# Performance work log

Hardware: AMD Instinct MI355X
Metric: run time of the kernel (lower is better)

The kernel has to match this reference:

```python
import jax, jax.numpy as jnp
import numpy as np

EPS = 1e-6
N_REP = 4  # num_heads // num_kv_heads


def _qk_norm(a):
    a32 = a.astype(jnp.float32)
    var = jnp.mean(jnp.square(a32), axis=-1, keepdims=True)
    return (a32 * jax.lax.rsqrt(var + EPS)).astype(a.dtype)


def setup_inputs() -> dict:
    key = jax.random.key(0)
    ks = jax.random.split(key, 5)
    B, Tq, C, H, D, Hkv = 2, 2048, 2048, 16, 128, 4
    s = 0.02
    return {
        "x_q": jax.random.normal(ks[0], (B, Tq, C), dtype=jnp.float32),
        "Wq": jax.random.normal(ks[1], (C, H, D), dtype=jnp.float32) * s,
        "Wk": jax.random.normal(ks[2], (C, Hkv, D), dtype=jnp.float32) * s,
        "Wv": jax.random.normal(ks[3], (C, Hkv, D), dtype=jnp.float32) * s,
        "Wo": jax.random.normal(ks[4], (H * D, C), dtype=jnp.float32) * s,
    }


def reference(x_q, Wq, Wk, Wv, Wo):
    # x_q: (B, Tq, C); self-attention (x_kv = x_q)
    B, Tq, C = x_q.shape
    D = Wq.shape[-1]
    q = jnp.einsum('btc,chd->bthd', x_q, Wq)   # (B,Tq,H,D)
    k = jnp.einsum('btc,chd->bthd', x_q, Wk)   # (B,Tq,Hkv,D)
    v = jnp.einsum('btc,chd->bthd', x_q, Wv)
    # per-head QK RMS-norm
    q = _qk_norm(q)
    k = _qk_norm(k)
    # GQA: repeat kv heads (each kv head repeated N_REP times consecutively)
    k = jnp.repeat(k, N_REP, axis=2)           # (B,Tq,H,D)
    v = jnp.repeat(v, N_REP, axis=2)
    scale = jnp.asarray(1.0 / np.sqrt(D), dtype=q.dtype)
    logits = jnp.einsum('bqhd,bkhd->bhqk', q, k) * scale
    attn = jax.nn.softmax(logits, axis=-1)
    out = jnp.einsum('bhqk,bkhd->bqhd', attn, v)
    out = out.reshape(B, Tq, -1)               # (B,Tq,H*D)
    return out @ Wo                            # (B,Tq,C)
```

## Files before the change

kernel.cpp:

```cpp
#include <hip/hip_runtime.h>

typedef __attribute__((ext_vector_type(4))) float f32x4;
typedef __attribute__((ext_vector_type(16))) float f32x16;
typedef __attribute__((ext_vector_type(8))) short bf16x8;
typedef __attribute__((ext_vector_type(4))) unsigned u32x4;

#define DEV __device__ __forceinline__

DEV unsigned short f2bf(float f) {
  unsigned u = __float_as_uint(f);
  unsigned r = (u + 0x7FFFu + ((u >> 16) & 1u)) >> 16;
  return (unsigned short)r;
}
DEV float bf2f(unsigned short h) { return __uint_as_float(((unsigned)h) << 16); }

DEV unsigned cvtpk(float lo, float hi) {
  unsigned r;
  asm("v_cvt_pk_bf16_f32 %0, %1, %2" : "=v"(r) : "v"(lo), "v"(hi));
  return r;
}
DEV bf16x8 frag4(unsigned a, unsigned b, unsigned c, unsigned d) {
  u32x4 u = {a, b, c, d};
  return __builtin_bit_cast(bf16x8, u);
}

typedef __attribute__((address_space(1))) void gas_t;
typedef __attribute__((address_space(3))) void las_t;
DEV void async16(void* lds, const void* g) {
  __builtin_amdgcn_global_load_lds((gas_t*)g, (las_t*)lds, 16, 0, 0);
}

__global__ void cast_x(const float* __restrict__ x, unsigned short* __restrict__ y, int n8) {
  int idx = blockIdx.x * blockDim.x + threadIdx.x;
  int stride = gridDim.x * blockDim.x;
  for (; idx < n8; idx += stride) {
    const float4* p = (const float4*)(x + (size_t)idx * 8);
    float4 v0 = p[0], v1 = p[1];
    bf16x8 o;
    o[0] = (short)f2bf(v0.x); o[1] = (short)f2bf(v0.y);
    o[2] = (short)f2bf(v0.z); o[3] = (short)f2bf(v0.w);
    o[4] = (short)f2bf(v1.x); o[5] = (short)f2bf(v1.y);
    o[6] = (short)f2bf(v1.z); o[7] = (short)f2bf(v1.w);
    *(bf16x8*)(y + (size_t)idx * 8) = o;
  }
}

__global__ void transpose_cast(const float* __restrict__ W, unsigned short* __restrict__ Wt,
                               int Kdim, int Nw) {
  __shared__ float tile[32][33];
  int n0 = blockIdx.x * 32, k0 = blockIdx.y * 32;
  int tx = threadIdx.x, ty = threadIdx.y;
#pragma unroll
  for (int r = ty; r < 32; r += 8)
    tile[r][tx] = W[(size_t)(k0 + r) * Nw + n0 + tx];
  __syncthreads();
#pragma unroll
  for (int r = ty; r < 32; r += 8)
    Wt[(size_t)(n0 + r) * Kdim + k0 + tx] = f2bf(tile[tx][r]);
}

template <int EPI>
__global__ __launch_bounds__(256, 2)
void gemm_bt(const unsigned short* __restrict__ A, const unsigned short* __restrict__ Bt,
             int Kr, float* __restrict__ Cf, int Nr,
             unsigned short* __restrict__ Qn, unsigned short* __restrict__ Kn,
             unsigned short* __restrict__ Vt) {
  __shared__ __align__(16) unsigned short lsA[128 * 32];
  __shared__ __align__(16) unsigned short lsB[128 * 32];
  const int t = threadIdx.x;
  const int lane = t & 63;
  const int w = t >> 6, wr = w >> 1, wc = w & 1;
  const int lo = lane & 15, hi = lane >> 4;
  const int m0 = blockIdx.y * 128, n0 = blockIdx.x * 128;

  const int c0 = t, c1 = t + 256;
  const unsigned short* gA0 = A + (size_t)(m0 + (c0 >> 2)) * Kr + (c0 & 3) * 8;
  const unsigned short* gA1 = A + (size_t)(m0 + (c1 >> 2)) * Kr + (c1 & 3) * 8;
  const unsigned short* gB0 = Bt + (size_t)(n0 + (c0 >> 2)) * Kr + (c0 & 3) * 8;
  const unsigned short* gB1 = Bt + (size_t)(n0 + (c1 >> 2)) * Kr + (c1 & 3) * 8;
  unsigned short* lA0 = lsA + c0 * 8;
  unsigned short* lA1 = lsA + c1 * 8;
  unsigned short* lB0 = lsB + c0 * 8;
  unsigned short* lB1 = lsB + c1 * 8;

  f32x4 acc[4][4] = {};

  for (int kt = 0; kt < Kr; kt += 32) {
    async16(lA0, gA0 + kt);
    async16(lA1, gA1 + kt);
    async16(lB0, gB0 + kt);
    async16(lB1, gB1 + kt);
    __syncthreads();
    bf16x8 af[4], bfr[4];
#pragma unroll
    for (int i = 0; i < 4; ++i) {
      af[i]  = *(const bf16x8*)&lsA[(wr * 64 + i * 16 + lo) * 32 + hi * 8];
      bfr[i] = *(const bf16x8*)&lsB[(wc * 64 + i * 16 + lo) * 32 + hi * 8];
    }
#pragma unroll
    for (int mi = 0; mi < 4; ++mi)
#pragma unroll
      for (int ni = 0; ni < 4; ++ni)
        acc[mi][ni] = __builtin_amdgcn_mfma_f32_16x16x32_bf16(af[mi], bfr[ni], acc[mi][ni], 0, 0, 0);
    __syncthreads();
  }

#pragma unroll
  for (int mi = 0; mi < 4; ++mi)
#pragma unroll
    for (int ni = 0; ni < 4; ++ni)
#pragma unroll
      for (int i = 0; i < 4; ++i) {
        int gm = m0 + wr * 64 + mi * 16 + hi * 4 + i;
        int gn = n0 + wc * 64 + ni * 16 + lo;
        float v = acc[mi][ni][i];
        if (EPI == 0) {
          Cf[(size_t)gm * Nr + gn] = v;
        } else {
          unsigned short bv = f2bf(v);
          int bb = gm >> 11, tt = gm & 2047;
          if (gn < 2048) {
            int hh = gn >> 7, dd = gn & 127;
            Qn[(((size_t)bb * 16 + hh) * 2048 + tt) * 128 + dd] = bv;
          } else if (gn < 2560) {
            int g2 = gn - 2048, hh = g2 >> 7, dd = g2 & 127;
            Kn[(((size_t)bb * 4 + hh) * 2048 + tt) * 128 + dd] = bv;
          } else {
            int g2 = gn - 2560, hh = g2 >> 7, dd = g2 & 127;
            Vt[(((size_t)bb * 4 + hh) * 128 + dd) * 2048 + tt] = bv;
          }
        }
      }
}

__global__ __launch_bounds__(256)
void qk_norm(unsigned short* __restrict__ Qn, unsigned short* __restrict__ Kn, float qscale) {
  int row = blockIdx.x * 4 + (threadIdx.x >> 6);
  int lane = threadIdx.x & 63;
  unsigned short* base;
  float scl;
  if (row < 65536) { base = Qn + (size_t)row * 128; scl = qscale; }
  else             { base = Kn + (size_t)(row - 65536) * 128; scl = 1.0f; }
  unsigned v = *(const unsigned*)(base + lane * 2);
  float a = bf2f((unsigned short)(v & 0xffffu));
  float b = bf2f((unsigned short)(v >> 16));
  float ss = a * a + b * b;
#pragma unroll
  for (int m = 1; m < 64; m <<= 1) ss += __shfl_xor(ss, m, 64);
  float r = rsqrtf(ss * (1.0f / 128.0f) + 1e-6f) * scl;
  *(unsigned*)(base + lane * 2) = ((unsigned)f2bf(b * r) << 16) | (unsigned)f2bf(a * r);
}

__global__ __launch_bounds__(256, 2)
void attn(const unsigned short* __restrict__ Q, const unsigned short* __restrict__ Kk,
          const unsigned short* __restrict__ Vt, unsigned short* __restrict__ AO) {
  const int bid = blockIdx.x;
  const int bh = (bid & 7) + 8 * (bid >> 7);
  const int qx = (bid >> 3) & 15;
  const int b = bh >> 4, h = bh & 15;
  const int hkv = h >> 2;
  const int t = threadIdx.x;
  const int w = t >> 6, lane = t & 63;
  const int qi = lane & 31, h1 = lane >> 5;
  const unsigned short* Qb = Q  + (size_t)bh * 2048 * 128;
  const unsigned short* Kb = Kk + (size_t)(b * 4 + hkv) * 2048 * 128;
  const unsigned short* Vb = Vt + (size_t)(b * 4 + hkv) * 128 * 2048;
  const int q0 = qx * 128 + w * 32;

  __shared__ __align__(16) unsigned short Klds[2][64 * 128];
  __shared__ __align__(16) unsigned short Vlds[2][128 * 64];

  bf16x8 qf[8];
#pragma unroll
  for (int s = 0; s < 8; ++s)
    qf[s] = *(const bf16x8*)&Qb[(size_t)(q0 + qi) * 128 + s * 16 + h1 * 8];

  f32x16 Oc[4] = {};
  float mrow = -1e30f, srow = 0.f;

#define STAGE_KV(bufi, kt_)                                                      \
  {                                                                              \
    const unsigned short* gK = Kb + (size_t)(kt_) * 128;                         \
    const unsigned short* gV = Vb + (kt_);                                       \
    _Pragma("unroll")                                                            \
    for (int j = 0; j < 4; ++j) {                                                \
      int gi = j * 256 + t;                                                      \
      int kr = gi >> 4, kg = (gi & 15) ^ (kr & 15);                              \
      async16(&Klds[bufi][gi * 8], gK + (size_t)kr * 128 + kg * 8);              \
      int vr = gi >> 3, vg = (gi & 7) ^ (vr & 7);                                \
      async16(&Vlds[bufi][gi * 8], gV + (size_t)vr * 2048 + vg * 8);             \
    }                                                                            \
  }

  STAGE_KV(0, 0);
  __syncthreads();

  int cur = 0;
  for (int kt = 0; kt < 2048; kt += 64) {
    if (kt + 64 < 2048) STAGE_KV(cur ^ 1, kt + 64);

    const unsigned short* KL = Klds[cur];
    const unsigned short* VL = Vlds[cur];

    f32x16 S[2] = {};
    __builtin_amdgcn_s_setprio(1);
#pragma unroll
    for (int mt = 0; mt < 2; ++mt) {
      const int krow = mt * 32 + qi;
      const unsigned short* krp = KL + krow * 128;
      const int rswz = krow & 15;
#pragma unroll
      for (int s = 0; s < 8; ++s) {
        bf16x8 kf = *(const bf16x8*)(krp + (((2 * s + h1) ^ rswz) << 3));
        S[mt] = __builtin_amdgcn_mfma_f32_32x32x16_bf16(kf, qf[s], S[mt], 0, 0, 0);
      }
    }
    __builtin_amdgcn_s_setprio(0);

    float t8[8];
#pragma unroll
    for (int r = 0; r < 8; ++r)
      t8[r] = fmaxf(fmaxf(S[0][r], S[0][r + 8]), fmaxf(S[1][r], S[1][r + 8]));
#pragma unroll
    for (int r = 0; r < 4; ++r) t8[r] = fmaxf(t8[r], t8[r + 4]);
    float mx = fmaxf(fmaxf(t8[0], t8[1]), fmaxf(t8[2], t8[3]));
    mx = fmaxf(mx, __shfl_xor(mx, 32, 64));
    if (__any(mx > mrow + 8.0f)) {
      float mnew = fmaxf(mrow, mx);
      float al = __builtin_amdgcn_exp2f(mrow - mnew);
      mrow = mnew;
      srow *= al;
#pragma unroll
      for (int dt = 0; dt < 4; ++dt)
#pragma unroll
        for (int r = 0; r < 16; ++r) Oc[dt][r] *= al;
    }
#pragma unroll
    for (int mt = 0; mt < 2; ++mt)
#pragma unroll
      for (int r = 0; r < 16; ++r)
        S[mt][r] = __builtin_amdgcn_exp2f(S[mt][r] - mrow);
    float s8[8];
#pragma unroll
    for (int r = 0; r < 8; ++r)
      s8[r] = (S[0][r] + S[0][r + 8]) + (S[1][r] + S[1][r + 8]);
#pragma unroll
    for (int r = 0; r < 4; ++r) s8[r] += s8[r + 4];
    float rs = (s8[0] + s8[1]) + (s8[2] + s8[3]);
    rs += __shfl_xor(rs, 32, 64);
    srow += rs;

    __builtin_amdgcn_s_setprio(1);
#pragma unroll
    for (int mt = 0; mt < 2; ++mt) {
      unsigned wd[8];
#pragma unroll
      for (int i2 = 0; i2 < 8; ++i2) wd[i2] = cvtpk(S[mt][2 * i2], S[mt][2 * i2 + 1]);
      unsigned r0 = __shfl_xor(h1 ? wd[0] : wd[2], 32, 64);
      unsigned r1 = __shfl_xor(h1 ? wd[1] : wd[3], 32, 64);
      unsigned r2 = __shfl_xor(h1 ? wd[4] : wd[6], 32, 64);
      unsigned r3 = __shfl_xor(h1 ? wd[5] : wd[7], 32, 64);
      bf16x8 pf0 = frag4(h1 ? r0 : wd[0], h1 ? r1 : wd[1], h1 ? wd[2] : r0, h1 ? wd[3] : r1);
      bf16x8 pf1 = frag4(h1 ? r2 : wd[4], h1 ? r3 : wd[5], h1 ? wd[6] : r2, h1 ? wd[7] : r3);
#pragma unroll
      for (int dt = 0; dt < 4; ++dt) {
        const int vrow = dt * 32 + qi;
        const unsigned short* vrp = VL + vrow * 64;
        const int vswz = vrow & 7;
        bf16x8 v0 = *(const bf16x8*)(vrp + (((mt * 4 + 0 + h1) ^ vswz) << 3));
        bf16x8 v1 = *(const bf16x8*)(vrp + (((mt * 4 + 2 + h1) ^ vswz) << 3));
        Oc[dt] = __builtin_amdgcn_mfma_f32_32x32x16_bf16(v0, pf0, Oc[dt], 0, 0, 0);
        Oc[dt] = __builtin_amdgcn_mfma_f32_32x32x16_bf16(v1, pf1, Oc[dt], 0, 0, 0);
      }
    }
    __builtin_amdgcn_s_setprio(0);

    __syncthreads();
    cur ^= 1;
  }

  const float inv = 1.0f / srow;
  const size_t orow = ((size_t)(b * 2048 + q0 + qi)) * 2048 + h * 128;
#pragma unroll
  for (int dt = 0; dt < 4; ++dt)
#pragma unroll
    for (int rq = 0; rq < 4; ++rq) {
      int d0 = dt * 32 + 8 * rq + 4 * h1;
      unsigned u0 = cvtpk(Oc[dt][4 * rq + 0] * inv, Oc[dt][4 * rq + 1] * inv);
      unsigned u1 = cvtpk(Oc[dt][4 * rq + 2] * inv, Oc[dt][4 * rq + 3] * inv);
      uint2 st = {u0, u1};
      *(uint2*)((unsigned short*)AO + orow + d0) = st;
    }
}

extern "C" void kernel_launch(void* const* d_in, const int* in_sizes, int n_in,
                              void* d_out, int out_size, void* d_ws, size_t ws_size,
                              hipStream_t stream) {
  const float* x_q = (const float*)d_in[0];
  const float* Wq  = (const float*)d_in[1];
  const float* Wk  = (const float*)d_in[2];
  const float* Wv  = (const float*)d_in[3];
  const float* Wo  = (const float*)d_in[4];
  float* out = (float*)d_out;

  char* ws = (char*)d_ws;
  unsigned short* Xb    = (unsigned short*)(ws);
  unsigned short* WqkvT = (unsigned short*)(ws + 16777216);
  unsigned short* WoT   = (unsigned short*)(ws + 29360128);
  unsigned short* Qn    = (unsigned short*)(ws + 37748736);
  unsigned short* Kn    = (unsigned short*)(ws + 54525952);
  unsigned short* Vt    = (unsigned short*)(ws + 58720256);
  unsigned short* AO    = Xb;

  cast_x<<<2048, 256, 0, stream>>>(x_q, Xb, (4096 * 2048) / 8);
  transpose_cast<<<dim3(2048 / 32, 2048 / 32), dim3(32, 8), 0, stream>>>(Wq, WqkvT, 2048, 2048);
  transpose_cast<<<dim3(512 / 32, 2048 / 32), dim3(32, 8), 0, stream>>>(Wk, WqkvT + 2048 * 2048, 2048, 512);
  transpose_cast<<<dim3(512 / 32, 2048 / 32), dim3(32, 8), 0, stream>>>(Wv, WqkvT + 2560 * 2048, 2048, 512);
  transpose_cast<<<dim3(2048 / 32, 2048 / 32), dim3(32, 8), 0, stream>>>(Wo, WoT, 2048, 2048);

  gemm_bt<1><<<dim3(3072 / 128, 4096 / 128), 256, 0, stream>>>(Xb, WqkvT, 2048, nullptr, 0, Qn, Kn, Vt);
  qk_norm<<<(65536 + 16384) / 4, 256, 0, stream>>>(Qn, Kn, 0.12751742f);
  attn<<<512, 256, 0, stream>>>(Qn, Kn, Vt, AO);
  gemm_bt<0><<<dim3(2048 / 128, 4096 / 128), 256, 0, stream>>>(AO, WoT, 2048, out, 2048,
                                                               nullptr, nullptr, nullptr);
}
```

Baseline: 240.4 us.

## Pre-arrange V into MFMA fragment layout and load directly from global

Adds a fragV kernel that rewrites V into per-lane MFMA fragment order, so the attention kernel reads V fragments straight from global memory into registers instead of staging them through LDS. The attention block mapping is also changed so the four query heads sharing one KV head run together, and the GEMM tiles are remapped with an XCD-aware swizzle. These aim to cut LDS traffic and improve L2 reuse. The cost is an extra kernel launch and pass over V, plus more register pressure and exposed global load latency in the attention loop.

Measured after the change: 255.9 us. 1.06x slower.

```diff
diff --git a/kernel.cpp b/kernel.cpp
--- a/kernel.cpp
+++ b/kernel.cpp
@@ -71,7 +71,10 @@
   const int lane = t & 63;
   const int w = t >> 6, wr = w >> 1, wc = w & 1;
   const int lo = lane & 15, hi = lane >> 4;
-  const int m0 = blockIdx.y * 128, n0 = blockIdx.x * 128;
+  const int nwg = gridDim.x * 32;
+  const int bid0 = blockIdx.y * gridDim.x + blockIdx.x;
+  const int sw = (bid0 & 7) * (nwg >> 3) + (bid0 >> 3);
+  const int m0 = (sw & 31) * 128, n0 = (sw >> 5) * 128;
 
   const int c0 = t, c1 = t + 256;
   const unsigned short* gA0 = A + (size_t)(m0 + (c0 >> 2)) * Kr + (c0 & 3) * 8;
@@ -151,24 +154,37 @@
   *(unsigned*)(base + lane * 2) = ((unsigned)f2bf(b * r) << 16) | (unsigned)f2bf(a * r);
 }
 
+__global__ __launch_bounds__(256)
+void fragV(const unsigned short* __restrict__ Vt, unsigned short* __restrict__ Vf) {
+  int tid = blockIdx.x * 256 + threadIdx.x;
+  int bhkv = tid >> 15, c = tid & 32767;
+  int lane = c & 63, tile = c >> 10, mid = (c >> 6) & 15;
+  int dt = mid >> 2, g2 = mid & 3;
+  int d = dt * 32 + (lane & 31);
+  int g = g2 * 2 + (lane >> 5);
+  int k0 = tile * 64 + g * 8;
+  const uint4* src = (const uint4*)(Vt + ((size_t)bhkv * 128 + d) * 2048 + k0);
+  uint4* dst = (uint4*)(Vf + (size_t)bhkv * 262144 + (size_t)c * 8);
+  *dst = *src;
+}
+
 __global__ __launch_bounds__(256, 2)
 void attn(const unsigned short* __restrict__ Q, const unsigned short* __restrict__ Kk,
-          const unsigned short* __restrict__ Vt, unsigned short* __restrict__ AO) {
+          const unsigned short* __restrict__ Vf, unsigned short* __restrict__ AO) {
   const int bid = blockIdx.x;
-  const int bh = (bid & 7) + 8 * (bid >> 7);
-  const int qx = (bid >> 3) & 15;
-  const int b = bh >> 4, h = bh & 15;
-  const int hkv = h >> 2;
+  const int x = bid & 7, r2 = bid >> 3;
+  const int h2 = r2 & 3, qx = r2 >> 2;
+  const int b = x >> 2, hkv = x & 3;
+  const int h = hkv * 4 + h2, bh = b * 16 + h, bhkv = b * 4 + hkv;
   const int t = threadIdx.x;
   const int w = t >> 6, lane = t & 63;
   const int qi = lane & 31, h1 = lane >> 5;
   const unsigned short* Qb = Q  + (size_t)bh * 2048 * 128;
-  const unsigned short* Kb = Kk + (size_t)(b * 4 + hkv) * 2048 * 128;
-  const unsigned short* Vb = Vt + (size_t)(b * 4 + hkv) * 128 * 2048;
+  const unsigned short* Kb = Kk + (size_t)bhkv * 2048 * 128;
+  const unsigned short* Vfb = Vf + (size_t)bhkv * 262144;
   const int q0 = qx * 128 + w * 32;
 
   __shared__ __align__(16) unsigned short Klds[2][64 * 128];
-  __shared__ __align__(16) unsigned short Vlds[2][128 * 64];
 
   bf16x8 qf[8];
 #pragma unroll
@@ -178,29 +194,35 @@
   f32x16 Oc[4] = {};
   float mrow = -1e30f, srow = 0.f;
 
-#define STAGE_KV(bufi, kt_)                                                      \
+#define STAGE_K(bufi, kt_)                                                       \
   {                                                                              \
     const unsigned short* gK = Kb + (size_t)(kt_) * 128;                         \
-    const unsigned short* gV = Vb + (kt_);                                       \
     _Pragma("unroll")                                                            \
     for (int j = 0; j < 4; ++j) {                                                \
       int gi = j * 256 + t;                                                      \
       int kr = gi >> 4, kg = (gi & 15) ^ (kr & 15);                              \
       async16(&Klds[bufi][gi * 8], gK + (size_t)kr * 128 + kg * 8);              \
-      int vr = gi >> 3, vg = (gi & 7) ^ (vr & 7);                                \
-      async16(&Vlds[bufi][gi * 8], gV + (size_t)vr * 2048 + vg * 8);             \
     }                                                                            \
   }
 
-  STAGE_KV(0, 0);
+  STAGE_K(0, 0);
   __syncthreads();
 
   int cur = 0;
-  for (int kt = 0; kt < 2048; kt += 64) {
-    if (kt + 64 < 2048) STAGE_KV(cur ^ 1, kt + 64);
+  for (int ti = 0; ti < 32; ++ti) {
+    if (ti + 1 < 32) STAGE_K(cur ^ 1, (ti + 1) * 64);
+
+    bf16x8 vf0[2][4], vf1[2][4];
+#pragma unroll
+    for (int mt = 0; mt < 2; ++mt)
+#pragma unroll
+      for (int dt = 0; dt < 4; ++dt) {
+        const unsigned short* vp = Vfb + ((size_t)((ti * 4 + dt) * 4 + mt * 2)) * 512 + lane * 8;
+        vf0[mt][dt] = *(const bf16x8*)(vp);
+        vf1[mt][dt] = *(const bf16x8*)(vp + 512);
+      }
 
     const unsigned short* KL = Klds[cur];
-    const unsigned short* VL = Vlds[cur];
 
     f32x16 S[2] = {};
     __builtin_amdgcn_s_setprio(1);
@@ -258,19 +280,14 @@
       for (int i2 = 0; i2 < 8; ++i2) wd[i2] = cvtpk(S[mt][2 * i2], S[mt][2 * i2 + 1]);
       unsigned r0 = __shfl_xor(h1 ? wd[0] : wd[2], 32, 64);
       unsigned r1 = __shfl_xor(h1 ? wd[1] : wd[3], 32, 64);
-      unsigned r2 = __shfl_xor(h1 ? wd[4] : wd[6], 32, 64);
+      unsigned r2_ = __shfl_xor(h1 ? wd[4] : wd[6], 32, 64);
       unsigned r3 = __shfl_xor(h1 ? wd[5] : wd[7], 32, 64);
       bf16x8 pf0 = frag4(h1 ? r0 : wd[0], h1 ? r1 : wd[1], h1 ? wd[2] : r0, h1 ? wd[3] : r1);
-      bf16x8 pf1 = frag4(h1 ? r2 : wd[4], h1 ? r3 : wd[5], h1 ? wd[6] : r2, h1 ? wd[7] : r3);
+      bf16x8 pf1 = frag4(h1 ? r2_ : wd[4], h1 ? r3 : wd[5], h1 ? wd[6] : r2_, h1 ? wd[7] : r3);
 #pragma unroll
       for (int dt = 0; dt < 4; ++dt) {
-        const int vrow = dt * 32 + qi;
-        const unsigned short* vrp = VL + vrow * 64;
-        const int vswz = vrow & 7;
-        bf16x8 v0 = *(const bf16x8*)(vrp + (((mt * 4 + 0 + h1) ^ vswz) << 3));
-        bf16x8 v1 = *(const bf16x8*)(vrp + (((mt * 4 + 2 + h1) ^ vswz) << 3));
-        Oc[dt] = __builtin_amdgcn_mfma_f32_32x32x16_bf16(v0, pf0, Oc[dt], 0, 0, 0);
-        Oc[dt] = __builtin_amdgcn_mfma_f32_32x32x16_bf16(v1, pf1, Oc[dt], 0, 0, 0);
+        Oc[dt] = __builtin_amdgcn_mfma_f32_32x32x16_bf16(vf0[mt][dt], pf0, Oc[dt], 0, 0, 0);
+        Oc[dt] = __builtin_amdgcn_mfma_f32_32x32x16_bf16(vf1[mt][dt], pf1, Oc[dt], 0, 0, 0);
       }
     }
     __builtin_amdgcn_s_setprio(0);
@@ -311,6 +328,7 @@
   unsigned short* Kn    = (unsigned short*)(ws + 54525952);
   unsigned short* Vt    = (unsigned short*)(ws + 58720256);
   unsigned short* AO    = Xb;
+  unsigned short* Vf    = WqkvT;
 
   cast_x<<<2048, 256, 0, stream>>>(x_q, Xb, (4096 * 2048) / 8);
   transpose_cast<<<dim3(2048 / 32, 2048 / 32), dim3(32, 8), 0, stream>>>(Wq, WqkvT, 2048, 2048);
@@ -320,7 +338,8 @@
 
   gemm_bt<1><<<dim3(3072 / 128, 4096 / 128), 256, 0, stream>>>(Xb, WqkvT, 2048, nullptr, 0, Qn, Kn, Vt);
   qk_norm<<<(65536 + 16384) / 4, 256, 0, stream>>>(Qn, Kn, 0.12751742f);
-  attn<<<512, 256, 0, stream>>>(Qn, Kn, Vt, AO);
+  fragV<<<1024, 256, 0, stream>>>(Vt, Vf);
+  attn<<<512, 256, 0, stream>>>(Qn, Kn, Vf, AO);
   gemm_bt<0><<<dim3(2048 / 128, 4096 / 128), 256, 0, stream>>>(AO, WoT, 2048, out, 2048,
                                                                nullptr, nullptr, nullptr);
 }
```

## Fuse QK RMS-norm into QKV GEMM epilogue and swizzle block mapping

Applied to the files above, without the earlier changes.

Removes the separate qk_norm kernel by computing per-row sums of squares in the QKV GEMM epilogue. A 128-wide output tile covers exactly one head, so the reduction uses lane shuffles plus a cross-wave LDS exchange, and the normalized, scaled values are written straight out as bf16. This drops a full read/write pass over Q and K plus one launch, and normalizes from fp32 accumulators instead of rounded bf16. It also adds an XCD-style block-index swizzle that remaps tiles across the grid for cache locality, at the cost of a hardcoded 32-row-tile assumption.

New measurement: 239.1 us. No clear change (-0.5%).

```diff
diff --git a/kernel.cpp b/kernel.cpp
--- a/kernel.cpp
+++ b/kernel.cpp
@@ -64,14 +64,17 @@
 void gemm_bt(const unsigned short* __restrict__ A, const unsigned short* __restrict__ Bt,
              int Kr, float* __restrict__ Cf, int Nr,
              unsigned short* __restrict__ Qn, unsigned short* __restrict__ Kn,
-             unsigned short* __restrict__ Vt) {
+             unsigned short* __restrict__ Vt, float qscale) {
   __shared__ __align__(16) unsigned short lsA[128 * 32];
   __shared__ __align__(16) unsigned short lsB[128 * 32];
   const int t = threadIdx.x;
   const int lane = t & 63;
   const int w = t >> 6, wr = w >> 1, wc = w & 1;
   const int lo = lane & 15, hi = lane >> 4;
-  const int m0 = blockIdx.y * 128, n0 = blockIdx.x * 128;
+  const int nwg = gridDim.x * 32;
+  const int bid0 = blockIdx.y * gridDim.x + blockIdx.x;
+  const int sw = (bid0 & 7) * (nwg >> 3) + (bid0 >> 3);
+  const int m0 = (sw & 31) * 128, n0 = (sw >> 5) * 128;
 
   const int c0 = t, c1 = t + 256;
   const unsigned short* gA0 = A + (size_t)(m0 + (c0 >> 2)) * Kr + (c0 & 3) * 8;
@@ -105,6 +108,42 @@
     __syncthreads();
   }
 
+  float rr[4][4];
+  if (EPI == 1 && n0 < 2560) {
+    const float scl = (n0 < 2048) ? qscale : 1.0f;
+    float p[4][4];
+#pragma unroll
+    for (int mi = 0; mi < 4; ++mi)
+#pragma unroll
+      for (int i = 0; i < 4; ++i) {
+        float s = 0.f;
+#pragma unroll
+        for (int ni = 0; ni < 4; ++ni) s += acc[mi][ni][i] * acc[mi][ni][i];
+        p[mi][i] = s;
+      }
+#pragma unroll
+    for (int off = 1; off < 16; off <<= 1)
+#pragma unroll
+      for (int mi = 0; mi < 4; ++mi)
+#pragma unroll
+        for (int i = 0; i < 4; ++i) p[mi][i] += __shfl_xor(p[mi][i], off, 64);
+    float* red = (float*)lsA;
+    if (lo == 0)
+#pragma unroll
+      for (int mi = 0; mi < 4; ++mi)
+#pragma unroll
+        for (int i = 0; i < 4; ++i)
+          red[(wr * 2 + wc) * 64 + mi * 16 + hi * 4 + i] = p[mi][i];
+    __syncthreads();
+#pragma unroll
+    for (int mi = 0; mi < 4; ++mi)
+#pragma unroll
+      for (int i = 0; i < 4; ++i) {
+        float tot = p[mi][i] + red[(wr * 2 + (wc ^ 1)) * 64 + mi * 16 + hi * 4 + i];
+        rr[mi][i] = rsqrtf(tot * (1.0f / 128.0f) + 1e-6f) * scl;
+      }
+  }
+
 #pragma unroll
   for (int mi = 0; mi < 4; ++mi)
 #pragma unroll
@@ -117,6 +156,7 @@
         if (EPI == 0) {
           Cf[(size_t)gm * Nr + gn] = v;
         } else {
+          if (n0 < 2560) v *= rr[mi][i];
           unsigned short bv = f2bf(v);
           int bb = gm >> 11, tt = gm & 2047;
           if (gn < 2048) {
@@ -131,24 +171,6 @@
           }
         }
       }
-}
-
-__global__ __launch_bounds__(256)
-void qk_norm(unsigned short* __restrict__ Qn, unsigned short* __restrict__ Kn, float qscale) {
-  int row = blockIdx.x * 4 + (threadIdx.x >> 6);
-  int lane = threadIdx.x & 63;
-  unsigned short* base;
-  float scl;
-  if (row < 65536) { base = Qn + (size_t)row * 128; scl = qscale; }
-  else             { base = Kn + (size_t)(row - 65536) * 128; scl = 1.0f; }
-  unsigned v = *(const unsigned*)(base + lane * 2);
-  float a = bf2f((unsigned short)(v & 0xffffu));
-  float b = bf2f((unsigned short)(v >> 16));
-  float ss = a * a + b * b;
-#pragma unroll
-  for (int m = 1; m < 64; m <<= 1) ss += __shfl_xor(ss, m, 64);
-  float r = rsqrtf(ss * (1.0f / 128.0f) + 1e-6f) * scl;
-  *(unsigned*)(base + lane * 2) = ((unsigned)f2bf(b * r) << 16) | (unsigned)f2bf(a * r);
 }
 
 __global__ __launch_bounds__(256, 2)
@@ -318,9 +340,9 @@
   transpose_cast<<<dim3(512 / 32, 2048 / 32), dim3(32, 8), 0, stream>>>(Wv, WqkvT + 2560 * 2048, 2048, 512);
   transpose_cast<<<dim3(2048 / 32, 2048 / 32), dim3(32, 8), 0, stream>>>(Wo, WoT, 2048, 2048);
 
-  gemm_bt<1><<<dim3(3072 / 128, 4096 / 128), 256, 0, stream>>>(Xb, WqkvT, 2048, nullptr, 0, Qn, Kn, Vt);
-  qk_norm<<<(65536 + 16384) / 4, 256, 0, stream>>>(Qn, Kn, 0.12751742f);
+  gemm_bt<1><<<dim3(3072 / 128, 4096 / 128), 256, 0, stream>>>(Xb, WqkvT, 2048, nullptr, 0,
+                                                               Qn, Kn, Vt, 0.12751742f);
   attn<<<512, 256, 0, stream>>>(Qn, Kn, Vt, AO);
   gemm_bt<0><<<dim3(2048 / 128, 4096 / 128), 256, 0, stream>>>(AO, WoT, 2048, out, 2048,
-                                                               nullptr, nullptr, nullptr);
-}
+                                                               nullptr, nullptr, nullptr, 0.f);
+}
```
